# Performance work log

Measured on AMD Instinct MI355X. Metric: run time of the kernel, lower is better.

The kernel has to match this reference:

```python
import jax, jax.numpy as jnp
import numpy as np

B, N, DM, DE, H, L = 4, 256, 128, 8, 2 and 2, 8  # placeholder, real values below
B, N, DM, DE, H, L = 4, 256, 128, 8, 8, 2
D = DM // H  # per-head dim = 16
INNER = H * D


def setup_inputs() -> dict:
    key = jax.random.key(0)
    ks = jax.random.split(key, 20)
    nodes = jax.random.normal(ks[0], (B, N, DM), dtype=jnp.float32)
    edges = jax.random.normal(ks[1], (B, N, N, DE), dtype=jnp.float32)
    adjacency = (jax.random.uniform(ks[2], (B, N, N)) < 0.1).astype(jnp.float32)
    s = 0.02
    p = {
        'Wq': jax.random.normal(ks[3], (L, DM, INNER)) * s,
        'bq': jnp.zeros((L, INNER)),
        'Wk': jax.random.normal(ks[4], (L, DM, INNER)) * s,
        'bk': jnp.zeros((L, INNER)),
        'Wv': jax.random.normal(ks[5], (L, DM, INNER)) * s,
        'bv': jnp.zeros((L, INNER)),
        'We': jax.random.normal(ks[6], (L, DE, INNER)) * s,
        'be': jnp.zeros((L, INNER)),
        'Wres': jax.random.normal(ks[7], (L, DM, DM)) * s,
        'bres': jnp.zeros((L, DM)),
        'Wgate': jax.random.normal(ks[8], (L, 3 * DM, 1)) * s,
        'ln_g': jnp.ones((L, DM)),
        'ln_b': jnp.zeros((L, DM)),
    }
    return {'nodes': nodes, 'edges': edges, 'adjacency': adjacency, **p}


def _adj_softmax(sim, adj):
    # Faithful to source: torch.mean(x, dim, keepdim=True)[0] indexes batch 0,
    # giving a (N,1) shift broadcast over all batch*head rows.
    means = jnp.mean(sim, axis=-1, keepdims=True)[0]
    x_exp = jnp.exp(sim - means) * adj
    s = jnp.sum(x_exp, axis=-1, keepdims=True)
    s = jnp.where(s == 0, 1.0, s)
    return x_exp / s


def reference(nodes, edges, adjacency, Wq, bq, Wk, bk, Wv, bv, We, be,
              Wres, bres, Wgate, ln_g, ln_b):
    b, n, dm = nodes.shape
    h, d = H, DM // H
    scale = 1.0 / jnp.sqrt(jnp.float32(d))
    adj = jnp.broadcast_to(adjacency[:, None], (b, h, n, n)).reshape(b * h, n, n)
    x = nodes
    for l in range(L):  # fixed small layer count
        def heads(t):  # (b,n,h*d) -> (b*h, n, d)
            return t.reshape(b, n, h, d).transpose(0, 2, 1, 3).reshape(b * h, n, d)
        q = heads(x @ Wq[l] + bq[l])
        k = heads(x @ Wk[l] + bk[l])
        v = heads(x @ Wv[l] + bv[l])
        # edge features: (b,n,n,h,d) -> (b*h, n, n, d)
        e = (edges @ We[l] + be[l]).reshape(b, n, n, h, d)
        e = e.transpose(0, 3, 1, 2, 4).reshape(b * h, n, n, d)
        ke = k[:, None, :, :] + e
        ve = v[:, None, :, :] + e
        sim = jnp.einsum('bid,bijd->bij', q, ke) * scale
        attn = _adj_softmax(sim, adj)
        out = jnp.einsum('bij,bijd->bid', attn, ve)
        out = out.reshape(b, h, n, d).transpose(0, 2, 1, 3).reshape(b, n, h * d)
        # GatedResidual
        res = x @ Wres[l] + bres[l]
        gate_in = jnp.concatenate([out, res, out - res], axis=-1)
        g = jax.nn.sigmoid(gate_in @ Wgate[l])
        y = out * g + res * (1 - g)
        mu = jnp.mean(y, axis=-1, keepdims=True)
        var = jnp.var(y, axis=-1, keepdims=True)
        y = (y - mu) / jnp.sqrt(var + 1e-5) * ln_g[l] + ln_b[l]
        x = jax.nn.relu(y)
    return x
```

## Files before the change

### kernel.cpp

```cpp
#include <hip/hip_runtime.h>

#define BB 4
#define NN 256
#define DMM 128
#define DEE 8
#define HH 8
#define DD 16
#define LAYERS 2
#define SCALE 0.25f
#define PS 260

struct Params {
  const float *nodes, *edges, *adjacency;
  const float *Wq, *bq, *Wk, *bk, *Wv, *bv, *We, *be, *Wres, *bres, *Wgate, *lng, *lnb;
  const float *src;
  float *x, *q, *k, *v, *res;
  float *out;
  int layer;
};

__global__ __launch_bounds__(256) void k_proj(Params P){
  const int t = threadIdx.x;
  const int m = t >> 6;
  const int cp = t & 63;
  const int row0 = blockIdx.x * 4;
  const int l = P.layer;
  const float *W, *bia; float* dst;
  if (m==0){ W = P.Wq + l*DMM*DMM; bia = P.bq + l*DMM; dst = P.q; }
  else if (m==1){ W = P.Wk + l*DMM*DMM; bia = P.bk + l*DMM; dst = P.k; }
  else if (m==2){ W = P.Wv + l*DMM*DMM; bia = P.bv + l*DMM; dst = P.v; }
  else { W = P.Wres + l*DMM*DMM; bia = P.bres + l*DMM; dst = P.res; }
  const float2 bv2 = *(const float2*)(bia + 2*cp);
  float acc0[4] = {bv2.x,bv2.x,bv2.x,bv2.x};
  float acc1[4] = {bv2.y,bv2.y,bv2.y,bv2.y};
  const float2* W2 = (const float2*)W;
  const float* xr = P.src + row0*DMM;
  #pragma unroll 8
  for (int kk=0; kk<DMM; kk++){
    float2 w = W2[kk*64+cp];
    #pragma unroll
    for (int r=0;r<4;r++){
      float xv = xr[r*DMM+kk];
      acc0[r] += xv*w.x; acc1[r] += xv*w.y;
    }
  }
  #pragma unroll
  for (int r=0;r<4;r++){
    *(float2*)(dst + (row0+r)*DMM + 2*cp) = make_float2(acc0[r], acc1[r]);
  }
}

__global__ __launch_bounds__(256) void k_attn(Params P){
  const int t = threadIdx.x;
  const int b = blockIdx.x >> 8;
  const int i = blockIdx.x & 255;
  const int l = P.layer;

  __shared__ float qs[128];
  __shared__ float qwe_s[64];
  __shared__ float qbe_s[8];
  __shared__ float es[8*PS];
  __shared__ float ps[8*PS];
  __shared__ float red_s[32];
  __shared__ float ssum_s[8];
  __shared__ float g_s[64];
  __shared__ float res_s[128];
  __shared__ float red_a[2], red_b[2], red_c[2];

  if (t < 128) qs[t] = P.q[(b*NN+i)*DMM + t];
  __syncthreads();
  if (t < 64){
    const int h = t>>3, c = t&7;
    const float* Wer = P.We + l*DEE*DMM + c*DMM + h*DD;
    float a = 0.f;
    #pragma unroll
    for (int d=0; d<DD; d++) a += qs[h*DD+d]*Wer[d];
    qwe_s[t] = a;
    if (c==0){
      const float* ber = P.be + l*DMM + h*DD;
      float a2 = 0.f;
      #pragma unroll
      for (int d=0; d<DD; d++) a2 += qs[h*DD+d]*ber[d];
      qbe_s[h] = a2;
    }
  }
  __syncthreads();

  {
    const int j = t;
    const float4* er4 = (const float4*)(P.edges + ((size_t)(b*NN+i)*NN + j)*DEE);
    float4 e0 = er4[0], e1 = er4[1];
    float ec[8] = {e0.x,e0.y,e0.z,e0.w, e1.x,e1.y,e1.z,e1.w};
    #pragma unroll
    for (int c=0;c<8;c++) es[c*PS+j] = ec[c];
    const float adj = P.adjacency[(size_t)(b*NN+i)*NN + j];
    const float4* kr = (const float4*)(P.k + (b*NN+j)*DMM);
    const float* qg = P.q + (b*NN+i)*DMM;
    float preg[8];
    #pragma unroll
    for (int h=0; h<HH; h++){
      float4 k0 = kr[h*4+0], k1 = kr[h*4+1], k2 = kr[h*4+2], k3 = kr[h*4+3];
      const float* qh = qg + h*DD;
      float sim = qbe_s[h];
      sim += qh[0]*k0.x + qh[1]*k0.y + qh[2]*k0.z + qh[3]*k0.w;
      sim += qh[4]*k1.x + qh[5]*k1.y + qh[6]*k1.z + qh[7]*k1.w;
      sim += qh[8]*k2.x + qh[9]*k2.y + qh[10]*k2.z + qh[11]*k2.w;
      sim += qh[12]*k3.x + qh[13]*k3.y + qh[14]*k3.z + qh[15]*k3.w;
      const float4* qw4 = (const float4*)(qwe_s + h*8);
      float4 wA = qw4[0], wB = qw4[1];
      sim += ec[0]*wA.x + ec[1]*wA.y + ec[2]*wA.z + ec[3]*wA.w;
      sim += ec[4]*wB.x + ec[5]*wB.y + ec[6]*wB.z + ec[7]*wB.w;
      sim *= SCALE;
      float p = __expf(sim) * adj;
      preg[h] = p;
      ps[h*PS+j] = p;
    }
    #pragma unroll
    for (int h=0; h<HH; h++){
      float v = preg[h];
      #pragma unroll
      for (int off=32; off; off>>=1) v += __shfl_xor(v, off, 64);
      if ((t&63)==0) red_s[(t>>6)*8 + h] = v;
    }
  }
  __syncthreads();

  float pv = 0.f;
  if (t < 128){
    const int h = t>>4, d = t&15;
    const float* vcol = P.v + b*NN*DMM + h*DD + d;
    const float4* pr = (const float4*)(ps + h*PS);
    #pragma unroll 4
    for (int jq=0; jq<64; jq++){
      float4 pp = pr[jq];
      const float* vv = vcol + jq*4*DMM;
      pv += pp.x*vv[0] + pp.y*vv[DMM] + pp.z*vv[2*DMM] + pp.w*vv[3*DMM];
    }
  } else if (t < 192){
    const int h = (t-128)>>3, c = (t-128)&7;
    const float4* pr = (const float4*)(ps + h*PS);
    const float4* er = (const float4*)(es + c*PS);
    float g = 0.f;
    #pragma unroll 4
    for (int jq=0; jq<64; jq++){
      float4 pp = pr[jq], ee = er[jq];
      g += pp.x*ee.x + pp.y*ee.y + pp.z*ee.z + pp.w*ee.w;
    }
    g_s[h*8+c] = g;
  } else {
    const int u = t - 192;
    const float2 rv = *(const float2*)(P.res + (b*NN+i)*DMM + 2*u);
    res_s[2*u] = rv.x; res_s[2*u+1] = rv.y;
    if (t >= 248){
      const int h = t - 248;
      ssum_s[h] = red_s[h] + red_s[8+h] + red_s[16+h] + red_s[24+h];
    }
  }
  __syncthreads();

  float o = 0.f, rr = 0.f;
  if (t < 128){
    const int h = t>>4;
    const float* Wec = P.We + l*DEE*DMM + t;
    float eacc = 0.f;
    #pragma unroll
    for (int c=0;c<8;c++) eacc += Wec[c*DMM] * g_s[h*8+c];
    const float ssum = ssum_s[h];
    const float denom = (ssum==0.f) ? 1.f : ssum;
    const float bev = P.be[l*DMM + t];
    o = (pv + eacc + ssum*bev) / denom;
    rr = res_s[t];
    const float* Wg = P.Wgate + l*3*DMM;
    float contrib = o*Wg[t] + rr*Wg[DMM+t] + (o-rr)*Wg[2*DMM+t];
    #pragma unroll
    for (int off=32; off; off>>=1) contrib += __shfl_xor(contrib, off, 64);
    if ((t&63)==0) red_a[t>>6] = contrib;
  }
  __syncthreads();

  float y = 0.f;
  if (t < 128){
    const float gs = red_a[0] + red_a[1];
    const float gate = 1.f/(1.f + __expf(-gs));
    y = o*gate + rr*(1.f-gate);
    float s1 = y, s2 = y*y;
    #pragma unroll
    for (int off=32; off; off>>=1){ s1 += __shfl_xor(s1, off, 64); s2 += __shfl_xor(s2, off, 64); }
    if ((t&63)==0){ red_b[t>>6] = s1; red_c[t>>6] = s2; }
  }
  __syncthreads();

  if (t < 128){
    const float mu  = (red_b[0]+red_b[1]) * (1.f/128.f);
    const float var = (red_c[0]+red_c[1]) * (1.f/128.f) - mu*mu;
    const float inv = rsqrtf(var + 1e-5f);
    float yn = (y - mu)*inv*P.lng[l*DMM+t] + P.lnb[l*DMM+t];
    yn = fmaxf(yn, 0.f);
    if (l == LAYERS-1) P.out[(b*NN+i)*DMM + t] = yn;
    else               P.x  [(b*NN+i)*DMM + t] = yn;
  }
}

extern "C" void kernel_launch(void* const* d_in, const int* in_sizes, int n_in,
                              void* d_out, int out_size, void* d_ws, size_t ws_size,
                              hipStream_t stream) {
  Params P;
  P.nodes     = (const float*)d_in[0];
  P.edges     = (const float*)d_in[1];
  P.adjacency = (const float*)d_in[2];
  P.Wq   = (const float*)d_in[3];  P.bq   = (const float*)d_in[4];
  P.Wk   = (const float*)d_in[5];  P.bk   = (const float*)d_in[6];
  P.Wv   = (const float*)d_in[7];  P.bv   = (const float*)d_in[8];
  P.We   = (const float*)d_in[9];  P.be   = (const float*)d_in[10];
  P.Wres = (const float*)d_in[11]; P.bres = (const float*)d_in[12];
  P.Wgate= (const float*)d_in[13];
  P.lng  = (const float*)d_in[14]; P.lnb  = (const float*)d_in[15];

  float* f = (float*)d_ws;
  const int S = BB*NN*DMM;
  P.x = f; P.q = f + S; P.k = f + 2*S; P.v = f + 3*S; P.res = f + 4*S;
  P.out = (float*)d_out;

  for (int l = 0; l < LAYERS; l++){
    P.layer = l;
    P.src = (l == 0) ? P.nodes : P.x;
    k_proj <<<256,  256, 0, stream>>>(P);
    k_attn <<<BB*NN,256, 0, stream>>>(P);
  }
}
```

Measured before the change: 158.0 us.

## Store V transposed for vectorized PV loads and move softmax row sums to idle threads

The projection kernel now writes V in a transposed (feature-major) layout, so the attention kernel's P·V loop can read contiguous float4 rows of V instead of doing strided scalar loads. The per-head softmax denominators are no longer computed with 8 wavefront shuffle reductions in the score phase. Instead, the otherwise lightly loaded threads 192-255 sum segments of the shared-memory probabilities, and the results are combined later. This shortens the score phase's critical path and improves coalescing, at the cost of strided transposed stores in the projection kernel.

```diff
diff --git a/kernel.cpp b/kernel.cpp
--- a/kernel.cpp
+++ b/kernel.cpp
@@ -14,7 +14,7 @@
   const float *nodes, *edges, *adjacency;
   const float *Wq, *bq, *Wk, *bk, *Wv, *bv, *We, *be, *Wres, *bres, *Wgate, *lng, *lnb;
   const float *src;
-  float *x, *q, *k, *v, *res;
+  float *x, *q, *k, *vt, *res;
   float *out;
   int layer;
 };
@@ -25,11 +25,11 @@
   const int cp = t & 63;
   const int row0 = blockIdx.x * 4;
   const int l = P.layer;
-  const float *W, *bia; float* dst;
-  if (m==0){ W = P.Wq + l*DMM*DMM; bia = P.bq + l*DMM; dst = P.q; }
-  else if (m==1){ W = P.Wk + l*DMM*DMM; bia = P.bk + l*DMM; dst = P.k; }
-  else if (m==2){ W = P.Wv + l*DMM*DMM; bia = P.bv + l*DMM; dst = P.v; }
-  else { W = P.Wres + l*DMM*DMM; bia = P.bres + l*DMM; dst = P.res; }
+  const float *W, *bia;
+  if (m==0){ W = P.Wq + l*DMM*DMM; bia = P.bq + l*DMM; }
+  else if (m==1){ W = P.Wk + l*DMM*DMM; bia = P.bk + l*DMM; }
+  else if (m==2){ W = P.Wv + l*DMM*DMM; bia = P.bv + l*DMM; }
+  else { W = P.Wres + l*DMM*DMM; bia = P.bres + l*DMM; }
   const float2 bv2 = *(const float2*)(bia + 2*cp);
   float acc0[4] = {bv2.x,bv2.x,bv2.x,bv2.x};
   float acc1[4] = {bv2.y,bv2.y,bv2.y,bv2.y};
@@ -44,9 +44,17 @@
       acc0[r] += xv*w.x; acc1[r] += xv*w.y;
     }
   }
-  #pragma unroll
-  for (int r=0;r<4;r++){
-    *(float2*)(dst + (row0+r)*DMM + 2*cp) = make_float2(acc0[r], acc1[r]);
+  if (m==2){
+    const int b = row0 >> 8, i0 = row0 & 255;
+    float* vtb = P.vt + b*DMM*NN;
+    *(float4*)(vtb + (2*cp  )*NN + i0) = make_float4(acc0[0],acc0[1],acc0[2],acc0[3]);
+    *(float4*)(vtb + (2*cp+1)*NN + i0) = make_float4(acc1[0],acc1[1],acc1[2],acc1[3]);
+  } else {
+    float* dst = (m==0) ? P.q : (m==1) ? P.k : P.res;
+    #pragma unroll
+    for (int r=0;r<4;r++){
+      *(float2*)(dst + (row0+r)*DMM + 2*cp) = make_float2(acc0[r], acc1[r]);
+    }
   }
 }
 
@@ -61,8 +69,7 @@
   __shared__ float qbe_s[8];
   __shared__ float es[8*PS];
   __shared__ float ps[8*PS];
-  __shared__ float red_s[32];
-  __shared__ float ssum_s[8];
+  __shared__ float red_s[64];
   __shared__ float g_s[64];
   __shared__ float res_s[128];
   __shared__ float red_a[2], red_b[2], red_c[2];
@@ -96,7 +103,6 @@
     const float adj = P.adjacency[(size_t)(b*NN+i)*NN + j];
     const float4* kr = (const float4*)(P.k + (b*NN+j)*DMM);
     const float* qg = P.q + (b*NN+i)*DMM;
-    float preg[8];
     #pragma unroll
     for (int h=0; h<HH; h++){
       float4 k0 = kr[h*4+0], k1 = kr[h*4+1], k2 = kr[h*4+2], k3 = kr[h*4+3];
@@ -111,16 +117,7 @@
       sim += ec[0]*wA.x + ec[1]*wA.y + ec[2]*wA.z + ec[3]*wA.w;
       sim += ec[4]*wB.x + ec[5]*wB.y + ec[6]*wB.z + ec[7]*wB.w;
       sim *= SCALE;
-      float p = __expf(sim) * adj;
-      preg[h] = p;
-      ps[h*PS+j] = p;
-    }
-    #pragma unroll
-    for (int h=0; h<HH; h++){
-      float v = preg[h];
-      #pragma unroll
-      for (int off=32; off; off>>=1) v += __shfl_xor(v, off, 64);
-      if ((t&63)==0) red_s[(t>>6)*8 + h] = v;
+      ps[h*PS+j] = __expf(sim) * adj;
     }
   }
   __syncthreads();
@@ -128,13 +125,13 @@
   float pv = 0.f;
   if (t < 128){
     const int h = t>>4, d = t&15;
-    const float* vcol = P.v + b*NN*DMM + h*DD + d;
+    const float4* vrow = (const float4*)(P.vt + b*DMM*NN + (h*DD+d)*NN);
     const float4* pr = (const float4*)(ps + h*PS);
     #pragma unroll 4
     for (int jq=0; jq<64; jq++){
       float4 pp = pr[jq];
-      const float* vv = vcol + jq*4*DMM;
-      pv += pp.x*vv[0] + pp.y*vv[DMM] + pp.z*vv[2*DMM] + pp.w*vv[3*DMM];
+      float4 vv = vrow[jq];
+      pv += pp.x*vv.x + pp.y*vv.y + pp.z*vv.z + pp.w*vv.w;
     }
   } else if (t < 192){
     const int h = (t-128)>>3, c = (t-128)&7;
@@ -151,10 +148,15 @@
     const int u = t - 192;
     const float2 rv = *(const float2*)(P.res + (b*NN+i)*DMM + 2*u);
     res_s[2*u] = rv.x; res_s[2*u+1] = rv.y;
-    if (t >= 248){
-      const int h = t - 248;
-      ssum_s[h] = red_s[h] + red_s[8+h] + red_s[16+h] + red_s[24+h];
-    }
+    const int h = u>>3, seg = u&7;
+    const float4* pr = (const float4*)(ps + h*PS + seg*32);
+    float s = 0.f;
+    #pragma unroll
+    for (int q8=0; q8<8; q8++){
+      float4 pp = pr[q8];
+      s += pp.x+pp.y+pp.z+pp.w;
+    }
+    red_s[u] = s;
   }
   __syncthreads();
 
@@ -165,7 +167,9 @@
     float eacc = 0.f;
     #pragma unroll
     for (int c=0;c<8;c++) eacc += Wec[c*DMM] * g_s[h*8+c];
-    const float ssum = ssum_s[h];
+    float ssum = 0.f;
+    #pragma unroll
+    for (int s8=0; s8<8; s8++) ssum += red_s[h*8+s8];
     const float denom = (ssum==0.f) ? 1.f : ssum;
     const float bev = P.be[l*DMM + t];
     o = (pv + eacc + ssum*bev) / denom;
@@ -218,7 +222,7 @@
 
   float* f = (float*)d_ws;
   const int S = BB*NN*DMM;
-  P.x = f; P.q = f + S; P.k = f + 2*S; P.v = f + 3*S; P.res = f + 4*S;
+  P.x = f; P.q = f + S; P.k = f + 2*S; P.vt = f + 3*S; P.res = f + 4*S;
   P.out = (float*)d_out;
 
   for (int l = 0; l < LAYERS; l++){
```

Result: slower. 170.7 us (+8.1%).
